# Performance work log

Hardware: AMD Instinct MI355X
Metric: run time of the kernel (lower is better)

Reference implementation:

```python
import jax, jax.numpy as jnp
import numpy as np

ALPHA = 0.01  # leaky_relu slope (forward default)

def _hist_entropy(x, bins):
    """Mean over batch of per-sample histogram entropy, matching
    np.histogram(sample, bins=bins) + entropy_calc(hist, bw=bins):
      H = -sum(p*log(p)) - log(1/bins) = -sum(p*log(p)) + log(bins).
    x: [B, D] float."""
    B, D = x.shape
    xmin = jnp.min(x, axis=1, keepdims=True)
    xmax = jnp.max(x, axis=1, keepdims=True)
    width = xmax - xmin
    safe_w = jnp.where(width > 0, width, 1.0)
    # np.histogram: equal-width bins over [min, max]; max value goes in last bin
    idx = jnp.floor((x - xmin) / safe_w * bins).astype(jnp.int32)
    idx = jnp.clip(idx, 0, bins - 1)
    flat = (jnp.arange(B, dtype=jnp.int32)[:, None] * bins + idx).reshape(-1)
    counts = jnp.zeros(B * bins, jnp.float32).at[flat].add(1.0).reshape(B, bins)
    p = counts / jnp.float32(D)
    plogp = jnp.where(p > 0, p * jnp.log(jnp.where(p > 0, p, 1.0)), 0.0)
    H = -jnp.sum(plogp, axis=1) + jnp.log(jnp.float32(bins))  # [B]
    return jnp.mean(H)

def _lin(x, W, b):
    return x @ W.T + b

def setup_inputs() -> dict:
    key = jax.random.key(0)
    ks = jax.random.split(key, 13)
    B = 65536
    dims = [(784, 256), (256, 128), (128, 128), (128, 128), (128, 32), (32, 10)]
    inp = {"x": jax.random.normal(ks[0], (B, 784), dtype=jnp.float32)}
    for i, (din, dout) in enumerate(dims):
        s = 1.0 / np.sqrt(din)
        inp[f"W{i+1}"] = jax.random.uniform(ks[1 + 2 * i], (dout, din), jnp.float32, -s, s)
        inp[f"b{i+1}"] = jax.random.uniform(ks[2 + 2 * i], (dout,), jnp.float32, -s, s)
    return inp

def reference(x, W1, b1, W2, b2, W3, b3, W4, b4, W5, b5, W6, b6):
    x = x.reshape(-1, 784)
    Hs = []
    for (W, b) in [(W1, b1), (W2, b2), (W3, b3), (W4, b4), (W5, b5)]:
        x = jax.nn.leaky_relu(_lin(x, W, b), ALPHA)
        Hs.append(_hist_entropy(x, x.shape[1]))  # bins = dim / bin_ratio(=1)
    x = jax.nn.relu(_lin(x, W6, b6))
    out = jax.nn.log_softmax(x, axis=1)
    return (out, Hs[0], Hs[1], Hs[2], Hs[3], Hs[4])
```

## Files before the change

kernel.cpp:

```cpp
#include <hip/hip_runtime.h>
#include <hip/hip_bf16.h>
#include <math.h>

#define ALPHA 0.01f

typedef __bf16 bf16x8 __attribute__((ext_vector_type(8)));
typedef float  floatx4 __attribute__((ext_vector_type(4)));

static __device__ __forceinline__ unsigned short f2bf_bits(float f) {
    return __builtin_bit_cast(unsigned short, (__bf16)f);
}

static __device__ __forceinline__ void glds16(const void* g, void* l) {
    __builtin_amdgcn_global_load_lds(
        (const __attribute__((address_space(1))) unsigned int*)g,
        (__attribute__((address_space(3))) unsigned int*)l, 16, 0, 0);
}

template <int CTRL>
static __device__ __forceinline__ float dppmov(float x) {
    int r = __builtin_amdgcn_update_dpp(0, __builtin_bit_cast(int, x), CTRL, 0xf, 0xf, false);
    return __builtin_bit_cast(float, r);
}
static __device__ __forceinline__ float red16min(float x) {
    x = fminf(x, dppmov<0x121>(x)); x = fminf(x, dppmov<0x122>(x));
    x = fminf(x, dppmov<0x124>(x)); x = fminf(x, dppmov<0x128>(x));
    return x;
}
static __device__ __forceinline__ float red16max(float x) {
    x = fmaxf(x, dppmov<0x121>(x)); x = fmaxf(x, dppmov<0x122>(x));
    x = fmaxf(x, dppmov<0x124>(x)); x = fmaxf(x, dppmov<0x128>(x));
    return x;
}
static __device__ __forceinline__ float red16sum(float x) {
    x += dppmov<0x121>(x); x += dppmov<0x122>(x);
    x += dppmov<0x124>(x); x += dppmov<0x128>(x);
    return x;
}
static __device__ __forceinline__ unsigned red16sumu(unsigned x) {
    x += (unsigned)__builtin_amdgcn_update_dpp(0, (int)x, 0x121, 0xf, 0xf, false);
    x += (unsigned)__builtin_amdgcn_update_dpp(0, (int)x, 0x122, 0xf, 0xf, false);
    x += (unsigned)__builtin_amdgcn_update_dpp(0, (int)x, 0x124, 0xf, 0xf, false);
    x += (unsigned)__builtin_amdgcn_update_dpp(0, (int)x, 0x128, 0xf, 0xf, false);
    return x;
}

static __device__ __forceinline__ uint4 pack8(float4 f0, float4 f1) {
    uint4 pk;
    pk.x = (unsigned)f2bf_bits(f0.x) | ((unsigned)f2bf_bits(f0.y) << 16);
    pk.y = (unsigned)f2bf_bits(f0.z) | ((unsigned)f2bf_bits(f0.w) << 16);
    pk.z = (unsigned)f2bf_bits(f1.x) | ((unsigned)f2bf_bits(f1.y) << 16);
    pk.w = (unsigned)f2bf_bits(f1.z) | ((unsigned)f2bf_bits(f1.w) << 16);
    return pk;
}

template <int DOUT>
static __device__ __forceinline__ float entropy_tile(const floatx4* acc,
        unsigned int* cc, int lane)
{
    constexpr int CTN   = DOUT / 16;
    constexpr int HALF  = DOUT / 2;
    constexpr int LOG2D = (DOUT == 256) ? 8 : (DOUT == 128) ? 7 : 5;
    constexpr float LOGB = (DOUT == 256) ? 5.54517744f
                         : (DOUT == 128) ? 4.85203026f : 3.46573590f;
    const int lane16 = lane & 15, q = lane >> 4;
    float Hq = 0.0f;
    #pragma unroll
    for (int reg = 0; reg < 4; reg++) {
        float mn = acc[0][reg], mx = mn;
        #pragma unroll
        for (int ct = 1; ct < CTN; ct++) {
            mn = fminf(mn, acc[ct][reg]);
            mx = fmaxf(mx, acc[ct][reg]);
        }
        mn = red16min(mn);
        mx = red16max(mx);
        float wdt = mx - mn;
        float scale = (float)DOUT / (wdt > 0.0f ? wdt : 1.0f);

        #pragma unroll
        for (int i = 0; i < DOUT / 32; i++) cc[lane16 + 16 * i] = 0u;

        unsigned hot = 0u;
        #pragma unroll
        for (int ct = 0; ct < CTN; ct++) {
            int b = (int)((acc[ct][reg] - mn) * scale);
            b = b < (DOUT - 1) ? b : (DOUT - 1);
            bool h = (b <= 2);
            hot += h ? (1u << (10 * b)) : 0u;
            if (!h) atomicAdd(&cc[b & (HALF - 1)],
                              1u << (((b >> (LOG2D - 1)) & 1) << 4));
        }
        hot = red16sumu(hot);
        if (lane16 == 0) {
            atomicAdd(&cc[0], hot & 0x3ffu);
            atomicAdd(&cc[1], (hot >> 10) & 0x3ffu);
            atomicAdd(&cc[2], hot >> 20);
        }

        float s = 0.0f;
        #pragma unroll
        for (int i = 0; i < DOUT / 32; i++) {
            unsigned int word = cc[lane16 + 16 * i];
            int c0 = (int)(word & 0xffffu), c1 = (int)(word >> 16);
            if (c0 > 0) { float p = (float)c0 * (1.0f / (float)DOUT); s += p * __logf(p); }
            if (c1 > 0) { float p = (float)c1 * (1.0f / (float)DOUT); s += p * __logf(p); }
        }
        s = red16sum(s);
        Hq += LOGB - s;
    }
    Hq += __shfl_xor(Hq, 16, 64);
    Hq += __shfl_xor(Hq, 32, 64);
    return Hq;
}

template <int DIN, int DOUT>
static __device__ __forceinline__ float tail_layer(const bf16x8* a,
    char* __restrict__ yt,
    const unsigned short* __restrict__ Wf, const float* __restrict__ bias,
    unsigned int* __restrict__ cc, int lane)
{
    constexpr int KT = DIN / 32, CTN = DOUT / 16, NCO = DOUT / 8;
    const int lane16 = lane & 15, q = lane >> 4;

    floatx4 acc[CTN];
    #pragma unroll
    for (int ct = 0; ct < CTN; ct++) acc[ct] = (floatx4)(bias[ct * 16 + lane16]);

    #pragma unroll
    for (int kt = 0; kt < KT; kt++) {
        #pragma unroll
        for (int ct = 0; ct < CTN; ct++) {
            bf16x8 bw = *(const bf16x8*)(Wf + ((size_t)(kt * CTN + ct) * 64 + lane) * 8);
            acc[ct] = __builtin_amdgcn_mfma_f32_16x16x32_bf16(a[kt], bw, acc[ct], 0, 0, 0);
        }
    }

    #pragma unroll
    for (int ct = 0; ct < CTN; ct++) {
        #pragma unroll
        for (int reg = 0; reg < 4; reg++) {
            float v = acc[ct][reg];
            v = v > 0.0f ? v : ALPHA * v;
            acc[ct][reg] = v;
            int r  = q * 4 + reg;
            int c  = (ct * 16 + lane16) >> 3;
            int cs = c ^ (r & (NCO - 1));
            *(unsigned short*)(yt + r * (DOUT * 2) + cs * 16 + (lane16 & 7) * 2)
                = f2bf_bits(v);
        }
    }
    return entropy_tile<DOUT>(acc, cc, lane);
}

template <int DIN>
static __device__ __forceinline__ void load_afrags(bf16x8* a,
    const char* __restrict__ yt, int lane16, int q)
{
    constexpr int KT = DIN / 32, NCI = DIN / 8;
    asm volatile("s_waitcnt lgkmcnt(0)" ::: "memory");
    #pragma unroll
    for (int kt = 0; kt < KT; kt++) {
        int cs = (kt * 4 + q) ^ (lane16 & (NCI - 1));
        a[kt] = *(const bf16x8*)(yt + lane16 * (DIN * 2) + cs * 16);
    }
    asm volatile("s_waitcnt lgkmcnt(0)" ::: "memory");
}

__global__ __launch_bounds__(256, 4) void mega(
    const float* __restrict__ X,
    const unsigned short* __restrict__ W1f, const float* __restrict__ b1,
    const unsigned short* __restrict__ W2f, const float* __restrict__ b2,
    const unsigned short* __restrict__ W3f, const float* __restrict__ b3,
    const unsigned short* __restrict__ W4f, const float* __restrict__ b4,
    const unsigned short* __restrict__ W5f, const float* __restrict__ b5,
    const float* __restrict__ W6, const float* __restrict__ b6,
    float* __restrict__ out, float* __restrict__ Hpart)
{
    __shared__ __align__(16) char region[32768];

    const int t = threadIdx.x;
    const int lane = t & 63, lane16 = lane & 15, q = lane >> 4, w = t >> 6;
    const int row0 = blockIdx.x * 64;
    const int myrow = w * 16 + lane16;
    const int hidx = blockIdx.x * 4 + w;

    floatx4 acc1[16];
    #pragma unroll
    for (int ct = 0; ct < 16; ct++) acc1[ct] = (floatx4)(b1[ct * 16 + lane16]);

    {
        auto stageW = [&](int kt2, char* buf) {
            #pragma unroll
            for (int i = 0; i < 4; i++)
                glds16(W1f + ((size_t)kt2 * 1024 + w * 256 + i * 64 + lane) * 8,
                       buf + (w * 256 + i * 64) * 16);
        };

        const float* Xr = X + (size_t)(row0 + myrow) * 784;

        stageW(0, region);
        float4 fa0 = *(const float4*)(Xr + q * 8);
        float4 fa1 = *(const float4*)(Xr + q * 8 + 4);
        asm volatile("s_waitcnt vmcnt(0) lgkmcnt(0)" ::: "memory");
        __builtin_amdgcn_s_barrier();

        #pragma unroll 1
        for (int kt = 0; kt < 24; kt++) {
            char* bufC = region + ((kt & 1) << 14);
            char* bufN = region + ((~kt & 1) << 14);
            stageW(kt + 1, bufN);

            bf16x8 a = __builtin_bit_cast(bf16x8, pack8(fa0, fa1));
            int noff = (kt == 23) ? ((q & 1) * 8) : (q * 8);
            const float* nsrc = Xr + (kt + 1) * 32 + noff;
            fa0 = *(const float4*)(nsrc);
            fa1 = *(const float4*)(nsrc + 4);

            #pragma unroll
            for (int ct = 0; ct < 16; ct++) {
                bf16x8 bw = *(const bf16x8*)(bufC + (ct * 64 + lane) * 16);
                acc1[ct] = __builtin_amdgcn_mfma_f32_16x16x32_bf16(a, bw, acc1[ct], 0, 0, 0);
            }
            asm volatile("s_waitcnt vmcnt(0) lgkmcnt(0)" ::: "memory");
            __builtin_amdgcn_s_barrier();
        }

        uint4 pk = pack8(fa0, fa1);
        if (q >= 2) { pk.x = 0u; pk.y = 0u; pk.z = 0u; pk.w = 0u; }
        bf16x8 a = __builtin_bit_cast(bf16x8, pk);
        #pragma unroll
        for (int ct = 0; ct < 16; ct++) {
            bf16x8 bw = *(const bf16x8*)(region + (ct * 64 + lane) * 16);
            acc1[ct] = __builtin_amdgcn_mfma_f32_16x16x32_bf16(a, bw, acc1[ct], 0, 0, 0);
        }
        asm volatile("s_waitcnt lgkmcnt(0)" ::: "memory");
        __builtin_amdgcn_s_barrier();
    }

    char* yt = region + w * 4096;
    unsigned int* cc = (unsigned int*)(region + 16384) + (w * 4 + q) * 129;

    #pragma unroll
    for (int ct = 0; ct < 16; ct++) {
        #pragma unroll
        for (int reg = 0; reg < 4; reg++) {
            float v = acc1[ct][reg];
            acc1[ct][reg] = v > 0.0f ? v : ALPHA * v;
        }
    }

    float H = entropy_tile<256>(acc1, cc, lane);
    if (lane == 0) Hpart[0 * 4096 + hidx] = H;

    bf16x8 a2[8];
    #pragma unroll
    for (int p = 0; p < 2; p++) {
        #pragma unroll
        for (int ct = 0; ct < 8; ct++) {
            #pragma unroll
            for (int reg = 0; reg < 4; reg++) {
                int r  = q * 4 + reg;
                int c  = (ct * 16 + lane16) >> 3;
                int cs = c ^ r;
                *(unsigned short*)(yt + r * 256 + cs * 16 + (lane16 & 7) * 2)
                    = f2bf_bits(acc1[p * 8 + ct][reg]);
            }
        }
        asm volatile("s_waitcnt lgkmcnt(0)" ::: "memory");
        #pragma unroll
        for (int kt = 0; kt < 4; kt++) {
            int cs = (kt * 4 + q) ^ lane16;
            a2[p * 4 + kt] = *(const bf16x8*)(yt + lane16 * 256 + cs * 16);
        }
        asm volatile("s_waitcnt lgkmcnt(0)" ::: "memory");
    }

    H = tail_layer<256, 128>(a2, yt, W2f, b2, cc, lane);
    if (lane == 0) Hpart[1 * 4096 + hidx] = H;

    bf16x8 a[4];
    load_afrags<128>(a, yt, lane16, q);
    H = tail_layer<128, 128>(a, yt, W3f, b3, cc, lane);
    if (lane == 0) Hpart[2 * 4096 + hidx] = H;

    load_afrags<128>(a, yt, lane16, q);
    H = tail_layer<128, 128>(a, yt, W4f, b4, cc, lane);
    if (lane == 0) Hpart[3 * 4096 + hidx] = H;

    load_afrags<128>(a, yt, lane16, q);
    H = tail_layer<128, 32>(a, yt, W5f, b5, cc, lane);
    if (lane == 0) Hpart[4 * 4096 + hidx] = H;

    asm volatile("s_waitcnt lgkmcnt(0)" ::: "memory");
    float x6[32];
    #pragma unroll
    for (int c = 0; c < 4; c++) {
        int cs = c ^ (lane16 & 3);
        bf16x8 v = *(const bf16x8*)(yt + lane16 * 64 + cs * 16);
        #pragma unroll
        for (int j = 0; j < 8; j++) x6[c * 8 + j] = (float)v[j];
    }

    float z[3];
    float m = -1e30f;
    #pragma unroll
    for (int s2 = 0; s2 < 3; s2++) {
        int jj = q * 3 + s2;
        float a6 = 0.0f;
        if (jj < 10) {
            a6 = b6[jj];
            #pragma unroll
            for (int k = 0; k < 32; k++) a6 = fmaf(x6[k], W6[jj * 32 + k], a6);
            a6 = fmaxf(a6, 0.0f);
            m = fmaxf(m, a6);
        }
        z[s2] = a6;
    }
    m = fmaxf(m, __shfl_xor(m, 16, 64));
    m = fmaxf(m, __shfl_xor(m, 32, 64));
    float se = 0.0f;
    #pragma unroll
    for (int s2 = 0; s2 < 3; s2++)
        if (q * 3 + s2 < 10) se += __expf(z[s2] - m);
    se += __shfl_xor(se, 16, 64);
    se += __shfl_xor(se, 32, 64);
    float ls = __logf(se);
    const size_t ro = (size_t)(row0 + w * 16 + lane16) * 10;
    #pragma unroll
    for (int s2 = 0; s2 < 3; s2++) {
        int jj = q * 3 + s2;
        if (jj < 10) out[ro + jj] = z[s2] - m - ls;
    }
}

__global__ void convert_wfrag(const float* __restrict__ W1, const float* __restrict__ W2,
                              const float* __restrict__ W3, const float* __restrict__ W4,
                              const float* __restrict__ W5, unsigned short* __restrict__ out)
{
    int s = blockIdx.x * 256 + threadIdx.x;
    if (s >= 34304) return;
    const float* W; int DIN, CTN, sl;
    if      (s < 25600) { W = W1; DIN = 784; CTN = 16; sl = s;         }
    else if (s < 29696) { W = W2; DIN = 256; CTN = 8;  sl = s - 25600; }
    else if (s < 31744) { W = W3; DIN = 128; CTN = 8;  sl = s - 29696; }
    else if (s < 33792) { W = W4; DIN = 128; CTN = 8;  sl = s - 31744; }
    else                { W = W5; DIN = 128; CTN = 2;  sl = s - 33792; }
    int kt = sl / (CTN * 64);
    int ct = (sl / 64) % CTN;
    int ln = sl & 63;
    int r  = ct * 16 + (ln & 15);
    int k0 = kt * 32 + (ln >> 4) * 8;
    unsigned short v[8];
    #pragma unroll
    for (int j = 0; j < 8; j++) {
        int k = k0 + j;
        v[j] = (k < DIN) ? f2bf_bits(W[(size_t)r * DIN + k]) : (unsigned short)0;
    }
    uint4 pk;
    pk.x = (unsigned)v[0] | ((unsigned)v[1] << 16);
    pk.y = (unsigned)v[2] | ((unsigned)v[3] << 16);
    pk.z = (unsigned)v[4] | ((unsigned)v[5] << 16);
    pk.w = (unsigned)v[6] | ((unsigned)v[7] << 16);
    *(uint4*)(out + (size_t)s * 8) = pk;
}

__global__ __launch_bounds__(256) void hreduce(const float* __restrict__ Hp,
                                               float* __restrict__ out_tail)
{
    __shared__ float sm[4];
    const int t = threadIdx.x, lane = t & 63, w = t >> 6;
    const int l = blockIdx.x;
    const float* p = Hp + (size_t)l * 4096;
    float s = 0.0f;
    for (int i = t; i < 4096; i += 256) s += p[i];
    #pragma unroll
    for (int off = 1; off <= 32; off <<= 1) s += __shfl_xor(s, off, 64);
    if (lane == 0) sm[w] = s;
    __syncthreads();
    if (t == 0)
        out_tail[l] = (sm[0] + sm[1] + sm[2] + sm[3]) * (1.0f / 65536.0f);
}

extern "C" void kernel_launch(void* const* d_in, const int* in_sizes, int n_in,
                              void* d_out, int out_size, void* d_ws, size_t ws_size,
                              hipStream_t stream)
{
    const float* x  = (const float*)d_in[0];
    const float* W1 = (const float*)d_in[1];  const float* b1 = (const float*)d_in[2];
    const float* W2 = (const float*)d_in[3];  const float* b2 = (const float*)d_in[4];
    const float* W3 = (const float*)d_in[5];  const float* b3 = (const float*)d_in[6];
    const float* W4 = (const float*)d_in[7];  const float* b4 = (const float*)d_in[8];
    const float* W5 = (const float*)d_in[9];  const float* b5 = (const float*)d_in[10];
    const float* W6 = (const float*)d_in[11]; const float* b6 = (const float*)d_in[12];
    float* out = (float*)d_out;

    constexpr int B = 65536;
    char* ws = (char*)d_ws;
    float* Hpart = (float*)ws;
    unsigned short* Wfrag = (unsigned short*)(ws + 81920);
    unsigned short* W1f = Wfrag;
    unsigned short* W2f = W1f + 25600 * 8;
    unsigned short* W3f = W2f + 4096 * 8;
    unsigned short* W4f = W3f + 2048 * 8;
    unsigned short* W5f = W4f + 2048 * 8;

    convert_wfrag<<<134, 256, 0, stream>>>(W1, W2, W3, W4, W5, Wfrag);

    mega<<<B / 64, 256, 0, stream>>>(
        x, W1f, b1, W2f, b2, W3f, b3, W4f, b4, W5f, b5, W6, b6, out, Hpart);

    hreduce<<<5, 256, 0, stream>>>(Hpart, out + (size_t)B * 10);
}
```

Before: 391.3 us.

## Stage W1 in half-tiles to shrink LDS and raise occupancy to 6 blocks

```diff
diff --git a/kernel.cpp b/kernel.cpp
--- a/kernel.cpp
+++ b/kernel.cpp
@@ -167,7 +167,7 @@
     asm volatile("s_waitcnt lgkmcnt(0)" ::: "memory");
 }
 
-__global__ __launch_bounds__(256, 4) void mega(
+__global__ __launch_bounds__(256, 6) void mega(
     const float* __restrict__ X,
     const unsigned short* __restrict__ W1f, const float* __restrict__ b1,
     const unsigned short* __restrict__ W2f, const float* __restrict__ b2,
@@ -177,7 +177,7 @@
     const float* __restrict__ W6, const float* __restrict__ b6,
     float* __restrict__ out, float* __restrict__ Hpart)
 {
-    __shared__ __align__(16) char region[32768];
+    __shared__ __align__(16) char region[24640];
 
     const int t = threadIdx.x;
     const int lane = t & 63, lane16 = lane & 15, q = lane >> 4, w = t >> 6;
@@ -190,49 +190,61 @@
     for (int ct = 0; ct < 16; ct++) acc1[ct] = (floatx4)(b1[ct * 16 + lane16]);
 
     {
-        auto stageW = [&](int kt2, char* buf) {
+        auto stageH = [&](int i) {
+            char* buf = region + ((i & 1) << 13);
             #pragma unroll
-            for (int i = 0; i < 4; i++)
-                glds16(W1f + ((size_t)kt2 * 1024 + w * 256 + i * 64 + lane) * 8,
-                       buf + (w * 256 + i * 64) * 16);
+            for (int j = 0; j < 2; j++)
+                glds16(W1f + ((size_t)(i * 512 + w * 128 + j * 64 + lane)) * 8,
+                       buf + (w * 128 + j * 64) * 16);
         };
 
         const float* Xr = X + (size_t)(row0 + myrow) * 784;
 
-        stageW(0, region);
+        stageH(0);
         float4 fa0 = *(const float4*)(Xr + q * 8);
         float4 fa1 = *(const float4*)(Xr + q * 8 + 4);
         asm volatile("s_waitcnt vmcnt(0) lgkmcnt(0)" ::: "memory");
         __builtin_amdgcn_s_barrier();
 
+        bf16x8 acur = __builtin_bit_cast(bf16x8, pack8(fa0, fa1));
+
         #pragma unroll 1
-        for (int kt = 0; kt < 24; kt++) {
-            char* bufC = region + ((kt & 1) << 14);
-            char* bufN = region + ((~kt & 1) << 14);
-            stageW(kt + 1, bufN);
-
-            bf16x8 a = __builtin_bit_cast(bf16x8, pack8(fa0, fa1));
-            int noff = (kt == 23) ? ((q & 1) * 8) : (q * 8);
-            const float* nsrc = Xr + (kt + 1) * 32 + noff;
-            fa0 = *(const float4*)(nsrc);
-            fa1 = *(const float4*)(nsrc + 4);
-
-            #pragma unroll
-            for (int ct = 0; ct < 16; ct++) {
-                bf16x8 bw = *(const bf16x8*)(bufC + (ct * 64 + lane) * 16);
-                acc1[ct] = __builtin_amdgcn_mfma_f32_16x16x32_bf16(a, bw, acc1[ct], 0, 0, 0);
+        for (int i = 0; i < 49; i++) {
+            stageH(i + 1);
+            const int kt = i >> 1;
+            if ((i & 1) == 0) {
+                int nk = kt + 1; if (nk > 24) nk = 24;
+                int noff = (nk == 24) ? ((q & 1) * 8) : (q * 8);
+                const float* nsrc = Xr + nk * 32 + noff;
+                fa0 = *(const float4*)(nsrc);
+                fa1 = *(const float4*)(nsrc + 4);
+            }
+            {
+                char* buf = region + ((i & 1) << 13);
+                const int cb = (i & 1) * 8;
+                #pragma unroll
+                for (int c = 0; c < 8; c++) {
+                    bf16x8 bw = *(const bf16x8*)(buf + (c * 64 + lane) * 16);
+                    acc1[cb + c] = __builtin_amdgcn_mfma_f32_16x16x32_bf16(
+                                       acur, bw, acc1[cb + c], 0, 0, 0);
+                }
+            }
+            if (i & 1) {
+                uint4 pk = pack8(fa0, fa1);
+                if (kt + 1 == 24 && q >= 2) { pk.x = 0u; pk.y = 0u; pk.z = 0u; pk.w = 0u; }
+                acur = __builtin_bit_cast(bf16x8, pk);
             }
             asm volatile("s_waitcnt vmcnt(0) lgkmcnt(0)" ::: "memory");
             __builtin_amdgcn_s_barrier();
         }
-
-        uint4 pk = pack8(fa0, fa1);
-        if (q >= 2) { pk.x = 0u; pk.y = 0u; pk.z = 0u; pk.w = 0u; }
-        bf16x8 a = __builtin_bit_cast(bf16x8, pk);
-        #pragma unroll
-        for (int ct = 0; ct < 16; ct++) {
-            bf16x8 bw = *(const bf16x8*)(region + (ct * 64 + lane) * 16);
-            acc1[ct] = __builtin_amdgcn_mfma_f32_16x16x32_bf16(a, bw, acc1[ct], 0, 0, 0);
+        {
+            char* buf = region + (1 << 13);
+            #pragma unroll
+            for (int c = 0; c < 8; c++) {
+                bf16x8 bw = *(const bf16x8*)(buf + (c * 64 + lane) * 16);
+                acc1[8 + c] = __builtin_amdgcn_mfma_f32_16x16x32_bf16(
+                                  acur, bw, acc1[8 + c], 0, 0, 0);
+            }
         }
         asm volatile("s_waitcnt lgkmcnt(0)" ::: "memory");
         __builtin_amdgcn_s_barrier();
```

Measured after the change: 1.034 ms. +164.2%, slower.
